# Kernel optimization log

Measured on AMD Instinct MI355X. Metric: run time of the kernel, lower is better.

## Reference

```python
import jax, jax.numpy as jnp
import numpy as np

B = 128          # graphs
N = 512          # nodes per graph
NT = B * N       # total nodes = 65536
E = NT * 16      # total edges = 1048576
IN = 64
H = 128
OUT = 2
L = 4            # num_layers
RATIO = 0.8


def setup_inputs() -> dict:
    key = jax.random.key(0)
    ks = jax.random.split(key, 20)

    def w(k, shape, fan_in):
        return jax.random.normal(k, shape, jnp.float32) / np.sqrt(fan_in)

    x = jax.random.normal(ks[0], (NT, IN), jnp.float32)
    edge_index = jax.random.randint(ks[1], (2, E), 0, NT, dtype=jnp.int32)
    batch = (jnp.arange(NT) // N).astype(jnp.int32)  # equal-size graphs

    return {
        "x": x,
        "edge_index": edge_index,
        "batch": batch,
        # conv1: GraphConv(IN, H, aggr='mean') -> lin_rel (w/ bias) + lin_root (no bias)
        "W1_rel": w(ks[2], (IN, H), IN),
        "W1_root": w(ks[3], (IN, H), IN),
        "b1": jnp.zeros((H,), jnp.float32),
        # convs[0..2]: GraphConv(H, H, aggr='mean'), stacked
        "Wc_rel": w(ks[4], (L - 1, H, H), H),
        "Wc_root": w(ks[5], (L - 1, H, H), H),
        "bc": jnp.zeros((L - 1, H), jnp.float32),
        # SAGPooling score GNN: GraphConv(H, 1) with default aggr='add'
        "pw_rel": w(ks[6], (H,), H),
        "pw_root": w(ks[7], (H,), H),
        "pb": jnp.zeros((1,), jnp.float32),
        # MLP head
        "lin1_W": w(ks[8], (L * H, H), L * H),
        "lin1_b": jnp.zeros((H,), jnp.float32),
        "lin2_W": w(ks[9], (H, OUT), H),
        "lin2_b": jnp.zeros((OUT,), jnp.float32),
    }


def _graph_conv_mean(x, src, dst, emask, W_rel, W_root, b, n):
    # PyG GraphConv: lin_rel(mean_{j->i} x_j) + lin_root(x_i); masked edges excluded.
    msg = x[src] * emask[:, None]                                  # [E, D] gather
    s = jax.ops.segment_sum(msg, dst, num_segments=n)              # [n, D] scatter-add
    cnt = jax.ops.segment_sum(emask, dst, num_segments=n)          # [n]
    agg = s / jnp.maximum(cnt, 1.0)[:, None]                       # zero for isolated nodes
    return agg @ W_rel + x @ W_root + b


def reference(x, edge_index, batch, W1_rel, W1_root, b1, Wc_rel, Wc_root, bc,
              pw_rel, pw_root, pb, lin1_W, lin1_b, lin2_W, lin2_b):
    src = edge_index[0]
    dst = edge_index[1]
    emask = jnp.ones((E,), jnp.float32)
    n = NT
    npg = N  # nodes per graph (all graphs equal size)

    h = jax.nn.relu(_graph_conv_mean(x, src, dst, emask, W1_rel, W1_root, b1, n))
    xs = [h.reshape(B, npg, H).mean(axis=1)]  # global_mean_pool

    for i in range(L - 1):
        h = jax.nn.relu(_graph_conv_mean(h, src, dst, emask, Wc_rel[i], Wc_root[i], bc[i], n))
        xs.append(h.reshape(B, npg, H).mean(axis=1))
        if i % 2 == 0 and i < L - 2:
            # ---- SAGPooling: score via GraphConv(H,1) with add aggregation ----
            smsg = jax.ops.segment_sum(h[src] * emask[:, None], dst, num_segments=n)
            score = smsg @ pw_rel + h @ pw_root + pb[0]            # [n]
            k = int(np.ceil(RATIO * npg))
            topv, topi = jax.lax.top_k(score.reshape(B, npg), k)   # per-graph top-k
            perm = (jnp.arange(B)[:, None] * npg + topi).reshape(-1)  # global kept ids
            h = h[perm] * jnp.tanh(topv.reshape(-1))[:, None]
            # remap edges; edges touching dropped nodes get masked out
            node_map = jnp.full((n,), -1, jnp.int32).at[perm].set(
                jnp.arange(B * k, dtype=jnp.int32))
            ns, nd = node_map[src], node_map[dst]
            keep = ((ns >= 0) & (nd >= 0)).astype(jnp.float32)
            emask = emask * keep
            src = jnp.where(ns >= 0, ns, 0)
            dst = jnp.where(nd >= 0, nd, 0)
            n = B * k
            npg = k

    xcat = jnp.concatenate(xs, axis=-1)                            # JumpingKnowledge 'cat'
    out = jax.nn.relu(xcat @ lin1_W + lin1_b)
    # dropout is identity in eval mode
    out = out @ lin2_W + lin2_b
    return jax.nn.log_softmax(out, axis=-1)
```

## Files before the change

### kernel.cpp

```cpp
#include <hip/hip_runtime.h>
#include <math.h>

#define NT 65536
#define EE 1048576
#define NB 128
#define KK 410
#define HH 128

typedef short bf16x8 __attribute__((ext_vector_type(8)));
typedef float f32x4 __attribute__((ext_vector_type(4)));
typedef unsigned int u32x4 __attribute__((ext_vector_type(4)));

__device__ __align__(16) unsigned short g_xbs[(size_t)8 * NT * 8];
__device__ __align__(16) unsigned short g_hs1[(size_t)8 * NT * 16];
__device__ __align__(16) unsigned short g_hgs[(size_t)8 * NT * 16];
__device__ __align__(16) unsigned short g_hb2[(size_t)NT * HH];
__device__ __align__(16) unsigned char  g_h8b[(size_t)8 * NT * 16];
__device__ __align__(16) unsigned short g_agg[(size_t)16 * NT * 8];
__device__ __align__(16) unsigned short g_wt1[128 * 128];
__device__ __align__(16) unsigned short g_wtc[3 * 128 * 256];
__device__ __align__(16) unsigned short g_csr1u[EE];
__device__ __align__(16) unsigned short g_csr2u[EE];
__device__ unsigned short g_keptu[NT];
__device__ unsigned int g_ebuck[EE];
__device__ int g_bcnt[128];
__device__ int g_bbase[129];
__device__ int g_bcur[128];
__device__ int g_kdeg[NT];
__device__ int g_perm1[NT];
__device__ int g_perm2[NT];
__device__ int g_rank1[NT];
__device__ int g_rank2[NT];
__device__ float g_trel[NT];
__device__ float g_troot[NT];
__device__ float g_gatef[NT];
__device__ float g_kinv[NT];
__device__ float g_xc4[4 * NB * 4 * 128];
__device__ int g_rows1[NT + 1];

__device__ __forceinline__ float b2f(unsigned short u) {
    union { unsigned int i; float f; } v;
    v.i = ((unsigned int)u) << 16;
    return v.f;
}
__device__ __forceinline__ unsigned short f2b(float f) {
    unsigned int x = __float_as_uint(f);
    unsigned int r = x + 0x7fffu + ((x >> 16) & 1u);
    return (unsigned short)(r >> 16);
}
__device__ __forceinline__ unsigned int pk2(float a, float b) {
    return (unsigned int)f2b(a) | ((unsigned int)f2b(b) << 16);
}
__device__ __forceinline__ unsigned int mul2(unsigned int wd, float g) {
    float lo = b2f((unsigned short)(wd & 0xffffu)) * g;
    float hi = b2f((unsigned short)(wd >> 16)) * g;
    return pk2(lo, hi);
}
__device__ __forceinline__ unsigned char enc8(float v) {
    v = fminf(v, 496.0f);
    unsigned int b = __float_as_uint(v * 0x1p-120f);
    unsigned int r = (b + 0x3ffffu + ((b >> 19) & 1u)) >> 19;
    return (unsigned char)r;
}
#define DEC8(u) ((u) ? __uint_as_float(((unsigned int)(u) << 19) + 0x3C000000u) : 0.0f)

__global__ void k_prep(const float* __restrict__ x,
                       const float* __restrict__ W1r, const float* __restrict__ W1o,
                       const float* __restrict__ Wcr, const float* __restrict__ Wco) {
    int tid = blockIdx.x * 256 + threadIdx.x;
    if (tid < 1048576) {
        float4 v = *(const float4*)&x[(size_t)tid * 4];
        unsigned int lo = pk2(v.x, v.y);
        unsigned int hi = pk2(v.z, v.w);
        int node = tid >> 4;
        int sl = (tid & 15) >> 1;
        int of = (tid & 1) * 4;
        *(uint2*)&g_xbs[(((size_t)sl) * NT + node) * 8 + of] = make_uint2(lo, hi);
    } else if (tid < 1048576 + 16384) {
        int r = tid - 1048576;
        int k = r & 127, n = r >> 7;
        float v = (k < 64) ? W1r[k * 128 + n] : W1o[(k - 64) * 128 + n];
        g_wt1[n * 128 + k] = f2b(v);
    } else if (tid < 1048576 + 16384 + 98304) {
        int r = tid - (1048576 + 16384);
        int l = r >> 15;
        int k = r & 255, n = (r >> 8) & 127;
        float v = (k < 128) ? Wcr[l * 16384 + k * 128 + n]
                            : Wco[l * 16384 + (k - 128) * 128 + n];
        g_wtc[l * 32768 + n * 256 + k] = f2b(v);
    } else if (tid < 1048576 + 16384 + 98304 + 128) {
        g_bcnt[tid - (1048576 + 16384 + 98304)] = 0;
    }
}

__global__ __launch_bounds__(256) void k_bhist(const int* __restrict__ dst) {
    __shared__ int h[128];
    if (threadIdx.x < 128) h[threadIdx.x] = 0;
    __syncthreads();
    int e0 = (blockIdx.x * 256 + threadIdx.x) * 4;
    int4 d = *(const int4*)&dst[e0];
    atomicAdd(&h[d.x >> 9], 1);
    atomicAdd(&h[d.y >> 9], 1);
    atomicAdd(&h[d.z >> 9], 1);
    atomicAdd(&h[d.w >> 9], 1);
    __syncthreads();
    if (threadIdx.x < 128 && h[threadIdx.x]) atomicAdd(&g_bcnt[threadIdx.x], h[threadIdx.x]);
}

__global__ __launch_bounds__(128) void k_bscan() {
    __shared__ int s[128];
    int t = threadIdx.x;
    int v = g_bcnt[t];
    s[t] = v;
    __syncthreads();
    for (int off = 1; off < 128; off <<= 1) {
        int u = (t >= off) ? s[t - off] : 0;
        __syncthreads();
        s[t] += u;
        __syncthreads();
    }
    g_bbase[t] = s[t] - v;
    g_bcur[t] = s[t] - v;
    if (t == 127) g_bbase[128] = s[127];
}

__global__ __launch_bounds__(256) void k_bscatter(const int* __restrict__ src,
                                                  const int* __restrict__ dst) {
    __shared__ int h[128];
    __shared__ int base[128];
    if (threadIdx.x < 128) h[threadIdx.x] = 0;
    __syncthreads();
    int e0 = (blockIdx.x * 256 + threadIdx.x) * 4;
    int4 s = *(const int4*)&src[e0];
    int4 d = *(const int4*)&dst[e0];
    int b0 = d.x >> 9, b1 = d.y >> 9, b2 = d.z >> 9, b3 = d.w >> 9;
    atomicAdd(&h[b0], 1);
    atomicAdd(&h[b1], 1);
    atomicAdd(&h[b2], 1);
    atomicAdd(&h[b3], 1);
    __syncthreads();
    if (threadIdx.x < 128) {
        int c = h[threadIdx.x];
        base[threadIdx.x] = c ? atomicAdd(&g_bcur[threadIdx.x], c) : 0;
        h[threadIdx.x] = 0;
    }
    __syncthreads();
    int r0 = atomicAdd(&h[b0], 1);
    g_ebuck[base[b0] + r0] = ((unsigned int)(d.x & 511) << 16) | (unsigned int)s.x;
    int r1 = atomicAdd(&h[b1], 1);
    g_ebuck[base[b1] + r1] = ((unsigned int)(d.y & 511) << 16) | (unsigned int)s.y;
    int r2 = atomicAdd(&h[b2], 1);
    g_ebuck[base[b2] + r2] = ((unsigned int)(d.z & 511) << 16) | (unsigned int)s.z;
    int r3 = atomicAdd(&h[b3], 1);
    g_ebuck[base[b3] + r3] = ((unsigned int)(d.w & 511) << 16) | (unsigned int)s.w;
}

__global__ __launch_bounds__(512) void k_bcsr() {
    __shared__ int hist[512];
    __shared__ int offs[512];
    __shared__ int cur[512];
    int g = blockIdx.x, t = threadIdx.x;
    hist[t] = 0;
    cur[t] = 0;
    __syncthreads();
    int b0 = g_bbase[g], b1 = g_bbase[g + 1];
    for (int e = b0 + t; e < b1; e += 512) {
        unsigned int p = g_ebuck[e];
        atomicAdd(&hist[p >> 16], 1);
    }
    __syncthreads();
    int v = hist[t];
    offs[t] = v;
    __syncthreads();
    for (int off = 1; off < 512; off <<= 1) {
        int u = (t >= off) ? offs[t - off] : 0;
        __syncthreads();
        offs[t] += u;
        __syncthreads();
    }
    int excl = offs[t] - v;
    g_rows1[g * 512 + t] = b0 + excl;
    if (t == 511) g_rows1[g * 512 + 512] = b0 + excl + v;
    __syncthreads();
    offs[t] = excl;
    __syncthreads();
    for (int e = b0 + t; e < b1; e += 512) {
        unsigned int p = g_ebuck[e];
        int dl = p >> 16;
        int r = atomicAdd(&cur[dl], 1);
        g_csr1u[b0 + offs[dl] + r] = (unsigned short)(p & 0xFFFFu);
    }
}

__global__ __launch_bounds__(512) void k_dperm() {
    __shared__ int h[64];
    __shared__ int base[64];
    int g = blockIdx.x, t = threadIdx.x;
    if (t < 64) h[t] = 0;
    __syncthreads();
    int n = g * 512 + t;
    int d = min(g_rows1[n + 1] - g_rows1[n], 63);
    atomicAdd(&h[d], 1);
    __syncthreads();
    if (t == 0) {
        int ss = 0;
#pragma unroll
        for (int i = 0; i < 64; i++) { base[i] = ss; ss += h[i]; }
    }
    __syncthreads();
    int pos = atomicAdd(&base[d], 1);
    g_perm1[g * 512 + pos] = n;
    g_rank1[n] = pos;
}

__global__ __launch_bounds__(512) void k_prune() {
    __shared__ int h[64];
    __shared__ int base[64];
    int g = blockIdx.x, t = threadIdx.x;
    int n = g * 512 + t;
    int r0 = g_rows1[n], r1 = g_rows1[n + 1];
    int kc = 0;
    for (int e = r0; e < r1; e++) {
        unsigned short sidx = g_csr1u[e];
        if (g_keptu[sidx]) { g_csr2u[r0 + kc] = sidx; kc++; }
    }
    g_kdeg[n] = kc;
    g_kinv[n] = 1.0f / (float)(kc > 0 ? kc : 1);
    if (t < 64) h[t] = 0;
    __syncthreads();
    int d = min(kc, 63);
    atomicAdd(&h[d], 1);
    __syncthreads();
    if (t == 0) {
        int ss = 0;
#pragma unroll
        for (int i = 0; i < 64; i++) { base[i] = ss; ss += h[i]; }
    }
    __syncthreads();
    int pos = atomicAdd(&base[d], 1);
    g_perm2[g * 512 + pos] = n;
    g_rank2[n] = pos;
}

template <int MODE>
__global__ __launch_bounds__(256) void k_agg() {
    int s = blockIdx.x & 7;
    int idx = (blockIdx.x >> 3) * 256 + threadIdx.x;
    int node = (MODE >= 2) ? g_perm2[idx] : g_perm1[idx];
    const unsigned short* csr = (MODE >= 2) ? g_csr2u : g_csr1u;
    int r0 = g_rows1[node];
    int r1 = (MODE >= 2) ? (r0 + g_kdeg[node]) : g_rows1[node + 1];
    float inv;
    if constexpr (MODE >= 2) {
        inv = g_kinv[node];
    } else {
        int c = r1 - r0;
        inv = 1.0f / (float)(c > 0 ? c : 1);
    }
    constexpr int NA = (MODE == 0) ? 8 : 16;
    float acc[NA];
#pragma unroll
    for (int i = 0; i < NA; i++) acc[i] = 0.f;

    const unsigned short* sp = nullptr;
    const unsigned char* sp8 = nullptr;
    if constexpr (MODE == 0) sp = g_xbs + (size_t)s * NT * 8;
    else if constexpr (MODE == 1) sp = g_hs1 + (size_t)s * NT * 16;
    else if constexpr (MODE == 2) sp = g_hgs + (size_t)s * NT * 16;
    else sp8 = g_h8b + (size_t)s * NT * 16;

#define ACCP(wd, J) { acc[J] += b2f((unsigned short)((wd) & 0xffffu)); acc[(J) + 1] += b2f((unsigned short)((wd) >> 16)); }
    auto body = [&](int ii) {
        if constexpr (MODE == 3) {
            uint4 w = *(const uint4*)&sp8[(size_t)ii * 16];
            acc[0] += DEC8(w.x & 0xffu);
            acc[1] += DEC8((w.x >> 8) & 0xffu);
            acc[2] += DEC8((w.x >> 16) & 0xffu);
            acc[3] += DEC8(w.x >> 24);
            acc[4] += DEC8(w.y & 0xffu);
            acc[5] += DEC8((w.y >> 8) & 0xffu);
            acc[6] += DEC8((w.y >> 16) & 0xffu);
            acc[7] += DEC8(w.y >> 24);
            acc[8] += DEC8(w.z & 0xffu);
            acc[9] += DEC8((w.z >> 8) & 0xffu);
            acc[10] += DEC8((w.z >> 16) & 0xffu);
            acc[11] += DEC8(w.z >> 24);
            acc[12] += DEC8(w.w & 0xffu);
            acc[13] += DEC8((w.w >> 8) & 0xffu);
            acc[14] += DEC8((w.w >> 16) & 0xffu);
            acc[15] += DEC8(w.w >> 24);
        } else if constexpr (MODE == 0) {
            uint4 v = *(const uint4*)&sp[(size_t)ii * 8];
            ACCP(v.x, 0) ACCP(v.y, 2) ACCP(v.z, 4) ACCP(v.w, 6)
        } else {
            uint4 v = *(const uint4*)&sp[(size_t)ii * 16];
            uint4 v2 = *(const uint4*)&sp[(size_t)ii * 16 + 8];
            ACCP(v.x, 0) ACCP(v.y, 2) ACCP(v.z, 4) ACCP(v.w, 6)
            ACCP(v2.x, 8) ACCP(v2.y, 10) ACCP(v2.z, 12) ACCP(v2.w, 14)
        }
    };
#undef ACCP

    int e = r0;
    for (; e < r1 && (e & 3); e++) body((int)csr[e]);
    for (; e + 4 <= r1; e += 4) {
        uint2 iv = *(const uint2*)&csr[e];
        body((int)(iv.x & 0xffffu));
        body((int)(iv.x >> 16));
        body((int)(iv.y & 0xffffu));
        body((int)(iv.y >> 16));
    }
    for (; e < r1; e++) body((int)csr[e]);

    u32x4 o;
    o[0] = pk2(acc[0] * inv, acc[1] * inv);
    o[1] = pk2(acc[2] * inv, acc[3] * inv);
    o[2] = pk2(acc[4] * inv, acc[5] * inv);
    o[3] = pk2(acc[6] * inv, acc[7] * inv);
    if constexpr (MODE == 0) {
        __builtin_nontemporal_store(o, (u32x4*)&g_agg[((size_t)s * NT + idx) * 8]);
    } else {
        __builtin_nontemporal_store(o, (u32x4*)&g_agg[((size_t)(2 * s) * NT + idx) * 8]);
        u32x4 o2;
        o2[0] = pk2(acc[8] * inv, acc[9] * inv);
        o2[1] = pk2(acc[10] * inv, acc[11] * inv);
        o2[2] = pk2(acc[12] * inv, acc[13] * inv);
        o2[3] = pk2(acc[14] * inv, acc[15] * inv);
        __builtin_nontemporal_store(o2, (u32x4*)&g_agg[((size_t)(2 * s + 1) * NT + idx) * 8]);
    }
}

__global__ __launch_bounds__(256) void k_gateS() {
    int tid = blockIdx.x * 256 + threadIdx.x;
    int n = tid >> 3, s = tid & 7;
    float g = g_gatef[n];
    const unsigned short* srcp = &g_hb2[(size_t)n * 128 + s * 16];
    uint4 a = *(const uint4*)srcp;
    uint4 b = *(const uint4*)(srcp + 8);
    uint4 oa, ob;
    oa.x = mul2(a.x, g); oa.y = mul2(a.y, g); oa.z = mul2(a.z, g); oa.w = mul2(a.w, g);
    ob.x = mul2(b.x, g); ob.y = mul2(b.y, g); ob.z = mul2(b.z, g); ob.w = mul2(b.w, g);
    unsigned short* d = &g_hgs[((size_t)s * NT + n) * 16];
    *(uint4*)d = oa;
    *(uint4*)(d + 8) = ob;
}

template <int KA, int KB, int MASKED, int DOTS, int ROOTK, int OUTK>
__global__ __launch_bounds__(256) void k_mm(int wsel, int wOfs, int rootSel, int rksel,
                                            const float* __restrict__ bias, int sec,
                                            const float* __restrict__ pwr,
                                            const float* __restrict__ pwt) {
    __shared__ float s[128];
    __shared__ unsigned short t16[(OUTK >= 2) ? 128 * 136 : 2];
    const unsigned short* Wt = (wsel ? g_wtc : g_wt1) + wOfs;
    const unsigned short* sb = (ROOTK == 1) ? (rootSel ? g_hgs : g_hs1) : g_xbs;
    const int* rankp = rksel ? g_rank2 : g_rank1;
    int rowbase = blockIdx.x * 128;
    const int K = KA + KB;
    int lane = threadIdx.x & 63;
    int w = threadIdx.x >> 6;
    int n16 = lane & 15, quad = lane >> 4;
    int rowloc = w * 32;
    int rowg = rowbase + rowloc;
    int g = blockIdx.x >> 2, qb = blockIdx.x & 3;
    int row0 = rowg + n16, row1 = rowg + 16 + n16;
    int ia0 = (row0 & ~511) | rankp[row0];
    int ia1 = (row1 & ~511) | rankp[row1];
    f32x4 acc[2][8];
#pragma unroll
    for (int rt = 0; rt < 2; rt++)
#pragma unroll
        for (int ct = 0; ct < 8; ct++)
#pragma unroll
            for (int i = 0; i < 4; i++) acc[rt][ct][i] = 0.f;

#pragma unroll
    for (int ks = 0; ks < K / 32; ks++) {
        int k0 = ks * 32;
        bf16x8 a0, a1;
        if (k0 < KA) {
            int fg = (k0 + quad * 8) >> 3;
            a0 = *(const bf16x8*)&g_agg[((size_t)fg * NT + ia0) * 8];
            a1 = *(const bf16x8*)&g_agg[((size_t)fg * NT + ia1) * 8];
        } else {
            int col = k0 - KA + quad * 8;
            if constexpr (ROOTK == 0) {
                int fg = col >> 3;
                a0 = *(const bf16x8*)&g_xbs[((size_t)fg * NT + row0) * 8];
                a1 = *(const bf16x8*)&g_xbs[((size_t)fg * NT + row1) * 8];
            } else {
                int fg = col >> 4, off = col & 15;
                a0 = *(const bf16x8*)&sb[((size_t)fg * NT + row0) * 16 + off];
                a1 = *(const bf16x8*)&sb[((size_t)fg * NT + row1) * 16 + off];
            }
        }
#pragma unroll
        for (int ct = 0; ct < 8; ct++) {
            bf16x8 b = *(const bf16x8*)&Wt[(size_t)(ct * 16 + n16) * K + k0 + quad * 8];
            acc[0][ct] = __builtin_amdgcn_mfma_f32_16x16x32_bf16(a0, b, acc[0][ct], 0, 0, 0);
            acc[1][ct] = __builtin_amdgcn_mfma_f32_16x16x32_bf16(a1, b, acc[1][ct], 0, 0, 0);
        }
    }

    if (threadIdx.x < 128) s[threadIdx.x] = 0.f;
#pragma unroll
    for (int rt = 0; rt < 2; rt++) {
        float m[4];
#pragma unroll
        for (int i = 0; i < 4; i++) {
            int r = rowg + rt * 16 + quad * 4 + i;
            m[i] = (!MASKED || g_keptu[r]) ? 1.0f : 0.0f;
        }
#pragma unroll
        for (int ct = 0; ct < 8; ct++) {
            int c = ct * 16 + n16;
            float bv = bias[c];
#pragma unroll
            for (int i = 0; i < 4; i++) {
                int r = rowg + rt * 16 + quad * 4 + i;
                float v = fmaxf(acc[rt][ct][i] + bv, 0.f) * m[i];
                acc[rt][ct][i] = v;
                if constexpr (OUTK == 1) g_hb2[(size_t)r * 128 + c] = f2b(v);
                if constexpr (OUTK >= 2) t16[(rowloc + rt * 16 + quad * 4 + i) * 136 + c] = f2b(v);
            }
        }
    }
    __syncthreads();

#pragma unroll
    for (int ct = 0; ct < 8; ct++) {
        float p = 0.f;
#pragma unroll
        for (int rt = 0; rt < 2; rt++)
#pragma unroll
            for (int i = 0; i < 4; i++) p += acc[rt][ct][i];
        p += __shfl_xor(p, 16);
        p += __shfl_xor(p, 32);
        if (quad == 0) atomicAdd(&s[ct * 16 + n16], p);
    }

    if (DOTS) {
        float pr[8], pt[8];
#pragma unroll
        for (int ct = 0; ct < 8; ct++) {
            pr[ct] = pwr[ct * 16 + n16];
            pt[ct] = pwt[ct * 16 + n16];
        }
#pragma unroll
        for (int rt = 0; rt < 2; rt++)
#pragma unroll
            for (int i = 0; i < 4; i++) {
                float dr = 0.f, dt = 0.f;
#pragma unroll
                for (int ct = 0; ct < 8; ct++) {
                    dr += acc[rt][ct][i] * pr[ct];
                    dt += acc[rt][ct][i] * pt[ct];
                }
                dr += __shfl_xor(dr, 1); dt += __shfl_xor(dt, 1);
                dr += __shfl_xor(dr, 2); dt += __shfl_xor(dt, 2);
                dr += __shfl_xor(dr, 4); dt += __shfl_xor(dt, 4);
                dr += __shfl_xor(dr, 8); dt += __shfl_xor(dt, 8);
                if (n16 == 0) {
                    int r = rowg + rt * 16 + quad * 4 + i;
                    g_trel[r] = dr;
                    g_troot[r] = dt;
                }
            }
    }
    __syncthreads();
    if (threadIdx.x < 128)
        g_xc4[((sec * NB + g) * 4 + qb) * 128 + threadIdx.x] = s[threadIdx.x];

    if constexpr (OUTK >= 2) {
        int tid = threadIdx.x;
#pragma unroll
        for (int rep = 0; rep < 8; rep++) {
            int chunk = rep * 256 + tid;
            int s_ = chunk >> 8, rem = chunk & 255;
            int nl = rem >> 1, hf = rem & 1;
            bf16x8 val = *(const bf16x8*)&t16[nl * 136 + s_ * 16 + hf * 8];
            *(bf16x8*)&g_hs1[((size_t)s_ * NT + rowbase + nl) * 16 + hf * 8] = val;
        }
        if constexpr (OUTK == 3) {
#pragma unroll
            for (int rep = 0; rep < 4; rep++) {
                int chunk = rep * 256 + tid;
                int s_ = chunk >> 7, nl = chunk & 127;
                const unsigned short* p = &t16[nl * 136 + s_ * 16];
                unsigned int wq[4];
#pragma unroll
                for (int q = 0; q < 4; q++) {
                    unsigned int c0 = enc8(b2f(p[q * 4 + 0]));
                    unsigned int c1 = enc8(b2f(p[q * 4 + 1]));
                    unsigned int c2 = enc8(b2f(p[q * 4 + 2]));
                    unsigned int c3 = enc8(b2f(p[q * 4 + 3]));
                    wq[q] = c0 | (c1 << 8) | (c2 << 16) | (c3 << 24);
                }
                *(uint4*)&g_h8b[((size_t)s_ * NT + rowbase + nl) * 16] =
                    make_uint4(wq[0], wq[1], wq[2], wq[3]);
            }
        }
    }
}

__global__ __launch_bounds__(256) void k_topk(const float* __restrict__ pb) {
    __shared__ float sv[512];
    __shared__ int si[512];
    int g = blockIdx.x, t = threadIdx.x;
    float pbv = pb[0];
    for (int l = t; l < 512; l += 256) {
        int node = g * 512 + l;
        int r0 = g_rows1[node], r1 = g_rows1[node + 1];
        float s = 0.f;
        int e = r0;
        for (; e + 4 <= r1; e += 4) {
            float s0 = g_trel[g_csr1u[e]];
            float s1 = g_trel[g_csr1u[e + 1]];
            float s2 = g_trel[g_csr1u[e + 2]];
            float s3 = g_trel[g_csr1u[e + 3]];
            s += (s0 + s1) + (s2 + s3);
        }
        for (; e < r1; e++) s += g_trel[g_csr1u[e]];
        sv[l] = s + g_troot[node] + pbv;
        si[l] = l;
    }
    __syncthreads();
    for (int k = 2; k <= 512; k <<= 1) {
        for (int j = k >> 1; j > 0; j >>= 1) {
            for (int i = t; i < 512; i += 256) {
                int p = i ^ j;
                if (p > i) {
                    float va = sv[i], vb = sv[p];
                    int ia = si[i], ib = si[p];
                    bool aFirst = (va > vb) || (va == vb && ia < ib);
                    bool up = ((i & k) == 0);
                    if (up != aFirst) { sv[i] = vb; sv[p] = va; si[i] = ib; si[p] = ia; }
                }
            }
            __syncthreads();
        }
    }
    for (int r = t; r < 512; r += 256) {
        int old = g * 512 + si[r];
        if (r < KK) {
            g_gatef[old] = tanhf(sv[r]);
            g_keptu[old] = 1;
        } else {
            g_gatef[old] = 0.f;
            g_keptu[old] = 0;
        }
    }
}

__global__ __launch_bounds__(128) void k_head(const float* __restrict__ W1, const float* __restrict__ b1,
                                              const float* __restrict__ W2, const float* __restrict__ b2,
                                              float* __restrict__ out) {
    __shared__ float xr[512];
    __shared__ float r0[128], r1[128];
    int g = blockIdx.x, t = threadIdx.x;
    for (int i = t; i < 512; i += 128) {
        int sec = i >> 7, c = i & 127;
        const float* p = &g_xc4[((sec * NB + g) * 4) * 128 + c];
        float v = p[0] + p[128] + p[256] + p[384];
        float inv = (sec < 2) ? (1.0f / 512.0f) : (1.0f / 410.0f);
        xr[i] = v * inv;
    }
    __syncthreads();
    float acc = b1[t];
    for (int k = 0; k < 512; k++) acc += xr[k] * W1[k * 128 + t];
    acc = fmaxf(acc, 0.f);
    r0[t] = acc * W2[t * 2 + 0];
    r1[t] = acc * W2[t * 2 + 1];
    __syncthreads();
    for (int off = 64; off > 0; off >>= 1) {
        if (t < off) { r0[t] += r0[t + off]; r1[t] += r1[t + off]; }
        __syncthreads();
    }
    if (t == 0) {
        float z0 = r0[0] + b2[0], z1 = r1[0] + b2[1];
        float m = fmaxf(z0, z1);
        float l = m + logf(expf(z0 - m) + expf(z1 - m));
        out[g * 2 + 0] = z0 - l;
        out[g * 2 + 1] = z1 - l;
    }
}

extern "C" void kernel_launch(void* const* d_in, const int* in_sizes, int n_in,
                              void* d_out, int out_size, void* d_ws, size_t ws_size,
                              hipStream_t stream) {
    const float* x = (const float*)d_in[0];
    const int* ei = (const int*)d_in[1];
    const int* src = ei;
    const int* dst = ei + EE;
    const float* W1r = (const float*)d_in[3];
    const float* W1o = (const float*)d_in[4];
    const float* b1 = (const float*)d_in[5];
    const float* Wcr = (const float*)d_in[6];
    const float* Wco = (const float*)d_in[7];
    const float* bc = (const float*)d_in[8];
    const float* pwr = (const float*)d_in[9];
    const float* pwt = (const float*)d_in[10];
    const float* pb = (const float*)d_in[11];
    const float* l1W = (const float*)d_in[12];
    const float* l1b = (const float*)d_in[13];
    const float* l2W = (const float*)d_in[14];
    const float* l2b = (const float*)d_in[15];
    float* out = (float*)d_out;

    k_prep<<<(1048576 + 16384 + 98304 + 128 + 255) / 256, 256, 0, stream>>>(x, W1r, W1o, Wcr, Wco);

    k_bhist<<<1024, 256, 0, stream>>>(dst);
    k_bscan<<<1, 128, 0, stream>>>();
    k_bscatter<<<1024, 256, 0, stream>>>(src, dst);
    k_bcsr<<<128, 512, 0, stream>>>();
    k_dperm<<<NB, 512, 0, stream>>>();

    k_agg<0><<<2048, 256, 0, stream>>>();
    k_mm<64, 64, 0, 0, 0, 2><<<512, 256, 0, stream>>>(0, 0, 0, 0, b1, 0, pwr, pwt);

    k_agg<1><<<2048, 256, 0, stream>>>();
    k_mm<128, 128, 0, 1, 1, 1><<<512, 256, 0, stream>>>(1, 0, 0, 0, bc, 1, pwr, pwt);

    k_topk<<<NB, 256, 0, stream>>>(pb);
    k_prune<<<NB, 512, 0, stream>>>();
    k_gateS<<<2048, 256, 0, stream>>>();

    k_agg<2><<<2048, 256, 0, stream>>>();
    k_mm<128, 128, 1, 0, 1, 3><<<512, 256, 0, stream>>>(1, 32768, 1, 1, bc + 128, 2, pwr, pwt);

    k_agg<3><<<2048, 256, 0, stream>>>();
    k_mm<128, 128, 1, 0, 1, 0><<<512, 256, 0, stream>>>(1, 65536, 0, 1, bc + 256, 3, pwr, pwt);

    k_head<<<NB, 128, 0, stream>>>(l1W, l1b, l2W, l2b, out);
}
```

Measured before the change: 550.1 us.

## Fuse degree-sort into CSR build, gating into prune, and pair-balance aggregation threads

Folds the degree-bucket permutation into k_bcsr, reusing the per-node degree already held in a register, and folds the gate-scaling pass into k_prune. This removes two kernel launches and one extra read of the row offsets. k_agg now runs half as many blocks. Each thread handles two nodes, one at position t and one at 511-t of the degree-sorted order, so short and long rows are paired and per-thread work evens out. The cost is fewer resident waves for hiding gather latency, and prune's 128 blocks now also do the gating work serially.

```diff
diff --git a/kernel.cpp b/kernel.cpp
--- a/kernel.cpp
+++ b/kernel.cpp
@@ -159,6 +159,7 @@
     __shared__ int hist[512];
     __shared__ int offs[512];
     __shared__ int cur[512];
+    __shared__ int db2[64];
     int g = blockIdx.x, t = threadIdx.x;
     hist[t] = 0;
     cur[t] = 0;
@@ -190,27 +191,21 @@
         int r = atomicAdd(&cur[dl], 1);
         g_csr1u[b0 + offs[dl] + r] = (unsigned short)(p & 0xFFFFu);
     }
-}
-
-__global__ __launch_bounds__(512) void k_dperm() {
-    __shared__ int h[64];
-    __shared__ int base[64];
-    int g = blockIdx.x, t = threadIdx.x;
-    if (t < 64) h[t] = 0;
-    __syncthreads();
-    int n = g * 512 + t;
-    int d = min(g_rows1[n + 1] - g_rows1[n], 63);
-    atomicAdd(&h[d], 1);
+    __syncthreads();
+    if (t < 64) hist[t] = 0;
+    __syncthreads();
+    int d = min(v, 63);
+    atomicAdd(&hist[d], 1);
     __syncthreads();
     if (t == 0) {
         int ss = 0;
 #pragma unroll
-        for (int i = 0; i < 64; i++) { base[i] = ss; ss += h[i]; }
-    }
-    __syncthreads();
-    int pos = atomicAdd(&base[d], 1);
-    g_perm1[g * 512 + pos] = n;
-    g_rank1[n] = pos;
+        for (int i = 0; i < 64; i++) { db2[i] = ss; ss += hist[i]; }
+    }
+    __syncthreads();
+    int pos = atomicAdd(&db2[d], 1);
+    g_perm1[g * 512 + pos] = g * 512 + t;
+    g_rank1[g * 512 + t] = pos;
 }
 
 __global__ __launch_bounds__(512) void k_prune() {
@@ -240,109 +235,117 @@
     int pos = atomicAdd(&base[d], 1);
     g_perm2[g * 512 + pos] = n;
     g_rank2[n] = pos;
+#pragma unroll
+    for (int rep = 0; rep < 8; rep++) {
+        int chunk = rep * 512 + t;
+        int nl = chunk >> 3, s = chunk & 7;
+        int nn = g * 512 + nl;
+        float gv = g_gatef[nn];
+        const unsigned short* srcp = &g_hb2[(size_t)nn * 128 + s * 16];
+        uint4 a = *(const uint4*)srcp;
+        uint4 b = *(const uint4*)(srcp + 8);
+        uint4 oa, ob;
+        oa.x = mul2(a.x, gv); oa.y = mul2(a.y, gv); oa.z = mul2(a.z, gv); oa.w = mul2(a.w, gv);
+        ob.x = mul2(b.x, gv); ob.y = mul2(b.y, gv); ob.z = mul2(b.z, gv); ob.w = mul2(b.w, gv);
+        unsigned short* dp = &g_hgs[((size_t)s * NT + nn) * 16];
+        *(uint4*)dp = oa;
+        *(uint4*)(dp + 8) = ob;
+    }
 }
 
 template <int MODE>
 __global__ __launch_bounds__(256) void k_agg() {
     int s = blockIdx.x & 7;
-    int idx = (blockIdx.x >> 3) * 256 + threadIdx.x;
-    int node = (MODE >= 2) ? g_perm2[idx] : g_perm1[idx];
+    int g = blockIdx.x >> 3;
+    int t = threadIdx.x;
+    int base = g * 512;
+    const int* perm = (MODE >= 2) ? g_perm2 : g_perm1;
     const unsigned short* csr = (MODE >= 2) ? g_csr2u : g_csr1u;
-    int r0 = g_rows1[node];
-    int r1 = (MODE >= 2) ? (r0 + g_kdeg[node]) : g_rows1[node + 1];
-    float inv;
-    if constexpr (MODE >= 2) {
-        inv = g_kinv[node];
-    } else {
-        int c = r1 - r0;
-        inv = 1.0f / (float)(c > 0 ? c : 1);
-    }
-    constexpr int NA = (MODE == 0) ? 8 : 16;
-    float acc[NA];
-#pragma unroll
-    for (int i = 0; i < NA; i++) acc[i] = 0.f;
-
     const unsigned short* sp = nullptr;
     const unsigned char* sp8 = nullptr;
     if constexpr (MODE == 0) sp = g_xbs + (size_t)s * NT * 8;
     else if constexpr (MODE == 1) sp = g_hs1 + (size_t)s * NT * 16;
     else if constexpr (MODE == 2) sp = g_hgs + (size_t)s * NT * 16;
     else sp8 = g_h8b + (size_t)s * NT * 16;
+    constexpr int NA = (MODE == 0) ? 8 : 16;
+
+#pragma unroll 1
+    for (int pass = 0; pass < 2; pass++) {
+        int idx = base + (pass ? (511 - t) : t);
+        int node = perm[idx];
+        int r0 = g_rows1[node];
+        int r1 = (MODE >= 2) ? (r0 + g_kdeg[node]) : g_rows1[node + 1];
+        float inv;
+        if constexpr (MODE >= 2) {
+            inv = g_kinv[node];
+        } else {
+            int c = r1 - r0;
+            inv = 1.0f / (float)(c > 0 ? c : 1);
+        }
+        float acc[NA];
+#pragma unroll
+        for (int i = 0; i < NA; i++) acc[i] = 0.f;
 
 #define ACCP(wd, J) { acc[J] += b2f((unsigned short)((wd) & 0xffffu)); acc[(J) + 1] += b2f((unsigned short)((wd) >> 16)); }
-    auto body = [&](int ii) {
-        if constexpr (MODE == 3) {
-            uint4 w = *(const uint4*)&sp8[(size_t)ii * 16];
-            acc[0] += DEC8(w.x & 0xffu);
-            acc[1] += DEC8((w.x >> 8) & 0xffu);
-            acc[2] += DEC8((w.x >> 16) & 0xffu);
-            acc[3] += DEC8(w.x >> 24);
-            acc[4] += DEC8(w.y & 0xffu);
-            acc[5] += DEC8((w.y >> 8) & 0xffu);
-            acc[6] += DEC8((w.y >> 16) & 0xffu);
-            acc[7] += DEC8(w.y >> 24);
-            acc[8] += DEC8(w.z & 0xffu);
-            acc[9] += DEC8((w.z >> 8) & 0xffu);
-            acc[10] += DEC8((w.z >> 16) & 0xffu);
-            acc[11] += DEC8(w.z >> 24);
-            acc[12] += DEC8(w.w & 0xffu);
-            acc[13] += DEC8((w.w >> 8) & 0xffu);
-            acc[14] += DEC8((w.w >> 16) & 0xffu);
-            acc[15] += DEC8(w.w >> 24);
-        } else if constexpr (MODE == 0) {
-            uint4 v = *(const uint4*)&sp[(size_t)ii * 8];
-            ACCP(v.x, 0) ACCP(v.y, 2) ACCP(v.z, 4) ACCP(v.w, 6)
+        auto body = [&](int ii) {
+            if constexpr (MODE == 3) {
+                uint4 w = *(const uint4*)&sp8[(size_t)ii * 16];
+                acc[0] += DEC8(w.x & 0xffu);
+                acc[1] += DEC8((w.x >> 8) & 0xffu);
+                acc[2] += DEC8((w.x >> 16) & 0xffu);
+                acc[3] += DEC8(w.x >> 24);
+                acc[4] += DEC8(w.y & 0xffu);
+                acc[5] += DEC8((w.y >> 8) & 0xffu);
+                acc[6] += DEC8((w.y >> 16) & 0xffu);
+                acc[7] += DEC8(w.y >> 24);
+                acc[8] += DEC8(w.z & 0xffu);
+                acc[9] += DEC8((w.z >> 8) & 0xffu);
+                acc[10] += DEC8((w.z >> 16) & 0xffu);
+                acc[11] += DEC8(w.z >> 24);
+                acc[12] += DEC8(w.w & 0xffu);
+                acc[13] += DEC8((w.w >> 8) & 0xffu);
+                acc[14] += DEC8((w.w >> 16) & 0xffu);
+                acc[15] += DEC8(w.w >> 24);
+            } else if constexpr (MODE == 0) {
+                uint4 v = *(const uint4*)&sp[(size_t)ii * 8];
+                ACCP(v.x, 0) ACCP(v.y, 2) ACCP(v.z, 4) ACCP(v.w, 6)
+            } else {
+                uint4 v = *(const uint4*)&sp[(size_t)ii * 16];
+                uint4 v2 = *(const uint4*)&sp[(size_t)ii * 16 + 8];
+                ACCP(v.x, 0) ACCP(v.y, 2) ACCP(v.z, 4) ACCP(v.w, 6)
+                ACCP(v2.x, 8) ACCP(v2.y, 10) ACCP(v2.z, 12) ACCP(v2.w, 14)
+            }
+        };
+#undef ACCP
+
+        int e = r0;
+        for (; e < r1 && (e & 3); e++) body((int)csr[e]);
+        for (; e + 4 <= r1; e += 4) {
+            uint2 iv = *(const uint2*)&csr[e];
+            body((int)(iv.x & 0xffffu));
+            body((int)(iv.x >> 16));
+            body((int)(iv.y & 0xffffu));
+            body((int)(iv.y >> 16));
+        }
+        for (; e < r1; e++) body((int)csr[e]);
+
+        u32x4 o;
+        o[0] = pk2(acc[0] * inv, acc[1] * inv);
+        o[1] = pk2(acc[2] * inv, acc[3] * inv);
+        o[2] = pk2(acc[4] * inv, acc[5] * inv);
+        o[3] = pk2(acc[6] * inv, acc[7] * inv);
+        if constexpr (MODE == 0) {
+            __builtin_nontemporal_store(o, (u32x4*)&g_agg[((size_t)s * NT + idx) * 8]);
         } else {
-            uint4 v = *(const uint4*)&sp[(size_t)ii * 16];
-            uint4 v2 = *(const uint4*)&sp[(size_t)ii * 16 + 8];
-            ACCP(v.x, 0) ACCP(v.y, 2) ACCP(v.z, 4) ACCP(v.w, 6)
-            ACCP(v2.x, 8) ACCP(v2.y, 10) ACCP(v2.z, 12) ACCP(v2.w, 14)
-        }
-    };
-#undef ACCP
-
-    int e = r0;
-    for (; e < r1 && (e & 3); e++) body((int)csr[e]);
-    for (; e + 4 <= r1; e += 4) {
-        uint2 iv = *(const uint2*)&csr[e];
-        body((int)(iv.x & 0xffffu));
-        body((int)(iv.x >> 16));
-        body((int)(iv.y & 0xffffu));
-        body((int)(iv.y >> 16));
-    }
-    for (; e < r1; e++) body((int)csr[e]);
-
-    u32x4 o;
-    o[0] = pk2(acc[0] * inv, acc[1] * inv);
-    o[1] = pk2(acc[2] * inv, acc[3] * inv);
-    o[2] = pk2(acc[4] * inv, acc[5] * inv);
-    o[3] = pk2(acc[6] * inv, acc[7] * inv);
-    if constexpr (MODE == 0) {
-        __builtin_nontemporal_store(o, (u32x4*)&g_agg[((size_t)s * NT + idx) * 8]);
-    } else {
-        __builtin_nontemporal_store(o, (u32x4*)&g_agg[((size_t)(2 * s) * NT + idx) * 8]);
-        u32x4 o2;
-        o2[0] = pk2(acc[8] * inv, acc[9] * inv);
-        o2[1] = pk2(acc[10] * inv, acc[11] * inv);
-        o2[2] = pk2(acc[12] * inv, acc[13] * inv);
-        o2[3] = pk2(acc[14] * inv, acc[15] * inv);
-        __builtin_nontemporal_store(o2, (u32x4*)&g_agg[((size_t)(2 * s + 1) * NT + idx) * 8]);
-    }
-}
-
-__global__ __launch_bounds__(256) void k_gateS() {
-    int tid = blockIdx.x * 256 + threadIdx.x;
-    int n = tid >> 3, s = tid & 7;
-    float g = g_gatef[n];
-    const unsigned short* srcp = &g_hb2[(size_t)n * 128 + s * 16];
-    uint4 a = *(const uint4*)srcp;
-    uint4 b = *(const uint4*)(srcp + 8);
-    uint4 oa, ob;
-    oa.x = mul2(a.x, g); oa.y = mul2(a.y, g); oa.z = mul2(a.z, g); oa.w = mul2(a.w, g);
-    ob.x = mul2(b.x, g); ob.y = mul2(b.y, g); ob.z = mul2(b.z, g); ob.w = mul2(b.w, g);
-    unsigned short* d = &g_hgs[((size_t)s * NT + n) * 16];
-    *(uint4*)d = oa;
-    *(uint4*)(d + 8) = ob;
+            __builtin_nontemporal_store(o, (u32x4*)&g_agg[((size_t)(2 * s) * NT + idx) * 8]);
+            u32x4 o2;
+            o2[0] = pk2(acc[8] * inv, acc[9] * inv);
+            o2[1] = pk2(acc[10] * inv, acc[11] * inv);
+            o2[2] = pk2(acc[12] * inv, acc[13] * inv);
+            o2[3] = pk2(acc[14] * inv, acc[15] * inv);
+            __builtin_nontemporal_store(o2, (u32x4*)&g_agg[((size_t)(2 * s + 1) * NT + idx) * 8]);
+        }
+    }
 }
 
 template <int KA, int KB, int MASKED, int DOTS, int ROOTK, int OUTK>
@@ -613,22 +616,20 @@
     k_bscan<<<1, 128, 0, stream>>>();
     k_bscatter<<<1024, 256, 0, stream>>>(src, dst);
     k_bcsr<<<128, 512, 0, stream>>>();
-    k_dperm<<<NB, 512, 0, stream>>>();
-
-    k_agg<0><<<2048, 256, 0, stream>>>();
+
+    k_agg<0><<<1024, 256, 0, stream>>>();
     k_mm<64, 64, 0, 0, 0, 2><<<512, 256, 0, stream>>>(0, 0, 0, 0, b1, 0, pwr, pwt);
 
-    k_agg<1><<<2048, 256, 0, stream>>>();
+    k_agg<1><<<1024, 256, 0, stream>>>();
     k_mm<128, 128, 0, 1, 1, 1><<<512, 256, 0, stream>>>(1, 0, 0, 0, bc, 1, pwr, pwt);
 
     k_topk<<<NB, 256, 0, stream>>>(pb);
     k_prune<<<NB, 512, 0, stream>>>();
-    k_gateS<<<2048, 256, 0, stream>>>();
-
-    k_agg<2><<<2048, 256, 0, stream>>>();
+
+    k_agg<2><<<1024, 256, 0, stream>>>();
     k_mm<128, 128, 1, 0, 1, 3><<<512, 256, 0, stream>>>(1, 32768, 1, 1, bc + 128, 2, pwr, pwt);
 
-    k_agg<3><<<2048, 256, 0, stream>>>();
+    k_agg<3><<<1024, 256, 0, stream>>>();
     k_mm<128, 128, 1, 0, 1, 0><<<512, 256, 0, stream>>>(1, 65536, 0, 1, bc + 256, 3, pwr, pwt);
 
     k_head<<<NB, 128, 0, stream>>>(l1W, l1b, l2W, l2b, out);
```

New measurement: 547.1 us. Within noise of the previous version (-0.5%).
